# Optimization experiments

Measured on AMD Instinct MI355X. Metric: run time of the kernel, lower is better.

## Reference

```python
import jax, jax.numpy as jnp
import numpy as np

B, C, N, K, OUT = 4, 128, 8192, 20, 128


def setup_inputs() -> dict:
    key = jax.random.key(0)
    k1, k2, k3 = jax.random.split(key, 3)
    x = jax.random.normal(k1, (B, C, N), dtype=jnp.float32)
    W = jax.random.normal(k2, (OUT, 2 * C), dtype=jnp.float32) * 0.02  # 1x1 conv weight over 2C edge channels
    b = jnp.zeros((OUT,), dtype=jnp.float32)
    return {"x": x, "W": W, "b": b}


def _knn_idx(x, k):
    # x: [B, C, N]; pairwise_distance = -||xi - xj||^2 (larger = closer)
    inner = -2.0 * jnp.einsum('bcn,bcm->bnm', x, x)          # [B,N,N]
    xx = jnp.sum(x * x, axis=1)                               # [B,N]
    pd = -xx[:, :, None] - inner - xx[:, None, :]             # [B,N,N]
    return jax.lax.top_k(pd, k)[1]                            # [B,N,k] int32


def reference(x, W, b):
    k = K
    idx = _knn_idx(x, k)                                      # [B,N,k]
    xt = jnp.transpose(x, (0, 2, 1))                          # [B,N,C]
    nbr = jax.vmap(lambda xb, ib: xb[ib])(xt, idx)            # [B,N,k,C] gather
    center = jnp.broadcast_to(xt[:, :, None, :], nbr.shape)   # [B,N,k,C]
    # torch: cat((x, x - feature), dim=3)
    edge = jnp.concatenate([center, center - nbr], axis=-1)   # [B,N,k,2C]
    # 1x1 Conv2d over channel dim + ReLU
    h = jnp.einsum('bnkc,oc->bonk', edge, W) + b[None, :, None, None]
    h = jax.nn.relu(h)
    # aggregate over neighbors (EdgeConv max pooling)
    return jnp.max(h, axis=-1)                                # [B,OUT,N]
```

## Files before the change

kernel.cpp:

```cpp
#include <hip/hip_runtime.h>
#include <float.h>

#define Bz   4
#define Cz   128
#define Nz   8192
#define Kz   20
#define OUTz 128

__global__ __launch_bounds__(256) void xx_kernel(const float* __restrict__ x,
                                                 float* __restrict__ xx) {
    int t = blockIdx.x * 256 + threadIdx.x;
    int b = t >> 13;
    int n = t & (Nz - 1);
    const float* xp = x + (size_t)b * Cz * Nz + n;
    float s = 0.f;
#pragma unroll 8
    for (int c = 0; c < Cz; ++c) {
        float v = xp[(size_t)c * Nz];
        s = fmaf(v, v, s);
    }
    xx[t] = s;
}

__global__ __launch_bounds__(256) void knn_kernel(const float* __restrict__ x,
                                                  const float* __restrict__ xxg,
                                                  int* __restrict__ idxout) {
    const int b  = blockIdx.y;
    const int q0 = blockIdx.x * 32;

    __shared__ __align__(16) float Ald[128 * 32];
    __shared__ __align__(16) float buf2[2 * 8 * 256];
    float* bufA = buf2;
    float* bufB = buf2 + 2048;
    float* sc   = buf2;

    const int tid  = threadIdx.x;
    const int tx   = tid & 31;
    const int ty   = tid >> 5;
    const int lane = tid & 63;
    const int wid  = tid >> 6;

    const float* xb = x + (size_t)b * Cz * Nz;

    {
        int q4 = (tid & 7) * 4;
        int c0 = tid >> 3;
#pragma unroll
        for (int rep = 0; rep < 4; ++rep) {
            int c = c0 + rep * 32;
            *(float4*)&Ald[c * 32 + q4] =
                *(const float4*)&xb[(size_t)c * Nz + q0 + q4];
        }
    }

    float tv[Kz];
    int   ti[Kz];
#pragma unroll
    for (int s = 0; s < Kz; ++s) { tv[s] = -FLT_MAX; ti[s] = 0; }
    float wv = -FLT_MAX;
    int wslot = 0;
    const int orow = wid * 8 + lane;
    const int srow = wid * 8 + (lane & 7);
    const int part = lane >> 3;

    float4 st0[2], st1[2];

#define LOADCHUNK(dst, kj, ch)                                                \
    {                                                                         \
        _Pragma("unroll")                                                     \
        for (int i = 0; i < 2; ++i)                                           \
            dst[i] = *(const float4*)&xb[(size_t)((ch) * 8 + ty) * Nz + (kj) + tx * 4 + i * 128]; \
    }

#define WRITECHUNK(src, buf)                                                  \
    {                                                                         \
        _Pragma("unroll")                                                     \
        for (int i = 0; i < 2; ++i)                                           \
            *(float4*)&(buf)[ty * 256 + tx * 4 + i * 128] = src[i];           \
    }

#define COMPUTECHUNK(buf, ch)                                                 \
    {                                                                         \
        _Pragma("unroll")                                                     \
        for (int cc = 0; cc < 8; ++cc) {                                      \
            float4 a0 = *(const float4*)&Ald[((ch) * 8 + cc) * 32 + ty * 4];  \
            float4 b0 = *(const float4*)&(buf)[cc * 256 + tx * 4];            \
            float4 b1 = *(const float4*)&(buf)[cc * 256 + 128 + tx * 4];      \
            float av[4] = {a0.x, a0.y, a0.z, a0.w};                           \
            float bv[8] = {b0.x, b0.y, b0.z, b0.w, b1.x, b1.y, b1.z, b1.w};   \
            _Pragma("unroll")                                                 \
            for (int q = 0; q < 4; ++q) {                                     \
                _Pragma("unroll")                                             \
                for (int k = 0; k < 8; ++k)                                   \
                    acc[q][k] = fmaf(av[q], bv[k], acc[q][k]);                \
            }                                                                 \
        }                                                                     \
    }

#define EXTRACT(pm_, gbase_)                                                  \
    {                                                                         \
        unsigned long long pm = (pm_);                                        \
        while (pm) {                                                          \
            int j = __ffsll(pm) - 1;                                          \
            pm &= pm - 1;                                                     \
            float s = sc[orow * 64 + ((j + 4 * orow) & 63)];                  \
            if (s > wv) {                                                     \
                int gj = (gbase_) + j;                                        \
                _Pragma("unroll")                                             \
                for (int s2 = 0; s2 < Kz; ++s2) {                             \
                    bool hit = (s2 == wslot);                                 \
                    tv[s2] = hit ? s : tv[s2];                                \
                    ti[s2] = hit ? gj : ti[s2];                               \
                }                                                             \
                wv = tv[0]; wslot = 0;                                        \
                _Pragma("unroll")                                             \
                for (int s2 = 1; s2 < Kz; ++s2)                               \
                    if (tv[s2] < wv) { wv = tv[s2]; wslot = s2; }             \
            }                                                                 \
        }                                                                     \
    }

    LOADCHUNK(st0, 0, 0);

#pragma unroll 1
    for (int kt = 0; kt < Nz / 256; ++kt) {
        const int kj0 = kt * 256;
        const int kjn = ((kt + 1) & (Nz / 256 - 1)) * 256;

        float acc[4][8];
#pragma unroll
        for (int q = 0; q < 4; ++q)
#pragma unroll
            for (int k = 0; k < 8; ++k) acc[q][k] = 0.f;

#pragma unroll 1
        for (int cp = 0; cp < 8; ++cp) {
            const int e = 2 * cp;
            WRITECHUNK(st0, bufA);
            __syncthreads();
            LOADCHUNK(st1, kj0, e + 1);
            COMPUTECHUNK(bufA, e);
            WRITECHUNK(st1, bufB);
            __syncthreads();
            if (e == 14) { LOADCHUNK(st0, kjn, 0); }
            else         { LOADCHUNK(st0, kj0, e + 2); }
            COMPUTECHUNK(bufB, e + 1);
        }
        __syncthreads();

        float4 xxlo = *(const float4*)&xxg[b * Nz + kj0 + tx * 4];
        float4 xxhi = *(const float4*)&xxg[b * Nz + kj0 + 128 + tx * 4];
        float xxa[8] = {xxlo.x, xxlo.y, xxlo.z, xxlo.w,
                        xxhi.x, xxhi.y, xxhi.z, xxhi.w};
        const int txh = tx >> 4;
        const int cl0 = (tx & 15) * 4;

#pragma unroll
        for (int h = 0; h < 4; ++h) {
            if (txh == (h & 1)) {
                const int qs = (h >> 1) * 4;
#pragma unroll
                for (int dq = 0; dq < 4; ++dq) {
                    int r = ty * 4 + dq;
                    float4 w;
                    w.x = 2.f * acc[dq][qs + 0] - xxa[qs + 0];
                    w.y = 2.f * acc[dq][qs + 1] - xxa[qs + 1];
                    w.z = 2.f * acc[dq][qs + 2] - xxa[qs + 2];
                    w.w = 2.f * acc[dq][qs + 3] - xxa[qs + 3];
                    *(float4*)&sc[r * 64 + ((cl0 + 4 * r) & 63)] = w;
                }
            }
            __syncthreads();

            float wvb = __shfl(wv, lane & 7);
            unsigned m = 0;
#pragma unroll
            for (int g = 0; g < 2; ++g) {
                int col = part * 8 + g * 4;
                float4 v = *(const float4*)&sc[srow * 64 + ((col + 4 * srow) & 63)];
                m |= (unsigned)(v.x > wvb) << (4 * g + 0);
                m |= (unsigned)(v.y > wvb) << (4 * g + 1);
                m |= (unsigned)(v.z > wvb) << (4 * g + 2);
                m |= (unsigned)(v.w > wvb) << (4 * g + 3);
            }
            unsigned long long f = (unsigned long long)m << (8 * part);
            f |= __shfl_xor(f, 8);
            f |= __shfl_xor(f, 16);
            f |= __shfl_xor(f, 32);
            if (lane < 8) { EXTRACT(f, kj0 + h * 64); }
            __syncthreads();
        }
    }

    if (lane < 8) {
        size_t base = ((size_t)b * Nz + q0 + orow) * Kz;
#pragma unroll
        for (int s = 0; s < Kz; ++s) idxout[base + s] = ti[s];
    }
#undef LOADCHUNK
#undef WRITECHUNK
#undef COMPUTECHUNK
#undef EXTRACT
}

__global__ __launch_bounds__(256) void feat_kernel(const float* __restrict__ x,
                                                   const float* __restrict__ W,
                                                   const float* __restrict__ bias,
                                                   float* __restrict__ Y) {
    const int gp0 = blockIdx.x * 64;
    const int b   = gp0 >> 13;
    const int n0  = gp0 & (Nz - 1);
    const int o0  = blockIdx.y * 64;

    __shared__ __align__(16) float xt[128 * 64];
    __shared__ __align__(16) float wt[128 * 64];

    const int tid = threadIdx.x;
    const int tx  = tid & 15;
    const int ty  = tid >> 4;

    {
        int li = tid & 63;
        int c0 = tid >> 6;
        const float* xbp = x + (size_t)b * Cz * Nz + n0;
#pragma unroll
        for (int rep = 0; rep < 32; ++rep) {
            int c = c0 + rep * 4;
            xt[c * 64 + li] = xbp[(size_t)c * Nz + li];
        }
    }
    {
        int lo = tid & 63;
        int c0 = tid >> 6;
        int oo = o0 + lo;
#pragma unroll
        for (int rep = 0; rep < 32; ++rep) {
            int c = c0 + rep * 4;
            float w;
            if (oo < 128) w = W[oo * 256 + c] + W[oo * 256 + 128 + c];
            else          w = W[(oo - 128) * 256 + 128 + c];
            wt[c * 64 + lo] = w;
        }
    }
    __syncthreads();

    float acc[4][4];
#pragma unroll
    for (int di = 0; di < 4; ++di)
#pragma unroll
        for (int dj = 0; dj < 4; ++dj) acc[di][dj] = 0.f;

    const int aoff = ty * 4;
    const int boff = tx * 4;
#pragma unroll 8
    for (int c = 0; c < 128; ++c) {
        float4 a  = *(const float4*)&xt[c * 64 + aoff];
        float4 ww = *(const float4*)&wt[c * 64 + boff];
        float av[4] = {a.x, a.y, a.z, a.w};
        float wvv[4] = {ww.x, ww.y, ww.z, ww.w};
#pragma unroll
        for (int di = 0; di < 4; ++di)
#pragma unroll
            for (int dj = 0; dj < 4; ++dj)
                acc[di][dj] = fmaf(av[di], wvv[dj], acc[di][dj]);
    }

    float4 bv = make_float4(0.f, 0.f, 0.f, 0.f);
    if (o0 < 128) bv = *(const float4*)&bias[o0 + tx * 4];
#pragma unroll
    for (int di = 0; di < 4; ++di) {
        float4 r;
        r.x = acc[di][0] + bv.x;
        r.y = acc[di][1] + bv.y;
        r.z = acc[di][2] + bv.z;
        r.w = acc[di][3] + bv.w;
        *(float4*)&Y[(size_t)(gp0 + ty * 4 + di) * 256 + o0 + tx * 4] = r;
    }
}

__global__ __launch_bounds__(256) void gather_kernel(const int* __restrict__ idxg,
                                                     const float* __restrict__ Y,
                                                     float* __restrict__ out) {
    const int gp0 = blockIdx.x * 64;
    const int b   = gp0 >> 13;
    const int n0  = gp0 & (Nz - 1);

    __shared__ int lidx[64 * 21];
    const int tid = threadIdx.x;
    for (int t = tid; t < 64 * Kz; t += 256) {
        int p = t / Kz, j = t - p * Kz;
        lidx[p * 21 + j] = idxg[(size_t)(gp0 + p) * Kz + j];
    }
    __syncthreads();

    const int p  = tid & 63;
    const int o0 = (tid >> 6) * 32;

    float mn[32];
#pragma unroll
    for (int q = 0; q < 32; ++q) mn[q] = FLT_MAX;

    for (int j = 0; j < Kz; ++j) {
        int m = lidx[p * 21 + j];
        const float4* vr =
            (const float4*)(Y + (size_t)(b * Nz + m) * 256 + 128 + o0);
#pragma unroll
        for (int q = 0; q < 8; ++q) {
            float4 v4 = vr[q];
            mn[4 * q + 0] = fminf(mn[4 * q + 0], v4.x);
            mn[4 * q + 1] = fminf(mn[4 * q + 1], v4.y);
            mn[4 * q + 2] = fminf(mn[4 * q + 2], v4.z);
            mn[4 * q + 3] = fminf(mn[4 * q + 3], v4.w);
        }
    }

    const float4* ur = (const float4*)(Y + (size_t)(gp0 + p) * 256 + o0);
#pragma unroll
    for (int q = 0; q < 8; ++q) {
        float4 u4 = ur[q];
        float r0 = fmaxf(u4.x - mn[4 * q + 0], 0.f);
        float r1 = fmaxf(u4.y - mn[4 * q + 1], 0.f);
        float r2 = fmaxf(u4.z - mn[4 * q + 2], 0.f);
        float r3 = fmaxf(u4.w - mn[4 * q + 3], 0.f);
        size_t ob = ((size_t)b * OUTz + o0 + 4 * q) * Nz + n0 + p;
        out[ob + 0 * Nz] = r0;
        out[ob + 1 * Nz] = r1;
        out[ob + 2 * Nz] = r2;
        out[ob + 3 * Nz] = r3;
    }
}

extern "C" void kernel_launch(void* const* d_in, const int* in_sizes, int n_in,
                              void* d_out, int out_size, void* d_ws, size_t ws_size,
                              hipStream_t stream) {
    const float* x    = (const float*)d_in[0];
    const float* W    = (const float*)d_in[1];
    const float* bias = (const float*)d_in[2];
    float* out = (float*)d_out;

    char* ws = (char*)d_ws;
    float* xx  = (float*)ws;
    int*   idx = (int*)(ws + (1 << 17));
    float* Y   = (float*)(ws + (4 << 20));

    xx_kernel<<<dim3(Bz * Nz / 256), dim3(256), 0, stream>>>(x, xx);

    knn_kernel<<<dim3(Nz / 32, Bz), dim3(256), 0, stream>>>(x, xx, idx);

    feat_kernel<<<dim3(Bz * Nz / 64, 4), dim3(256), 0, stream>>>(x, W, bias, Y);

    gather_kernel<<<dim3(Bz * Nz / 64), dim3(256), 0, stream>>>(idx, Y, out);
}
```

Before: 1.579 ms.

## Stream query features via scalar loads and compute distances per-thread without LDS tiling

Rewrites the kNN distance GEMM so each thread owns one key and accumulates dot products against all 32 queries. Query values are fetched into scalar registers with inline s_load_dwordx16, double-buffered across channels, and key values are loaded straight from global memory into VGPRs. This removes the LDS staging buffers and the per-chunk __syncthreads, and moves operand broadcast onto the scalar unit. In exchange each query value is now used for only one FMA per thread, reuse of key loads is lost, the inline asm waitcnt scheduling is fragile, and register pressure rises.

```diff
diff --git a/kernel.cpp b/kernel.cpp
--- a/kernel.cpp
+++ b/kernel.cpp
@@ -6,6 +6,8 @@
 #define Nz   8192
 #define Kz   20
 #define OUTz 128
+
+typedef float f16v __attribute__((ext_vector_type(16)));
 
 __global__ __launch_bounds__(256) void xx_kernel(const float* __restrict__ x,
                                                  float* __restrict__ xx) {
@@ -28,30 +30,14 @@
     const int b  = blockIdx.y;
     const int q0 = blockIdx.x * 32;
 
-    __shared__ __align__(16) float Ald[128 * 32];
-    __shared__ __align__(16) float buf2[2 * 8 * 256];
-    float* bufA = buf2;
-    float* bufB = buf2 + 2048;
-    float* sc   = buf2;
+    __shared__ float sc[32 * 64];
 
     const int tid  = threadIdx.x;
-    const int tx   = tid & 31;
-    const int ty   = tid >> 5;
     const int lane = tid & 63;
     const int wid  = tid >> 6;
 
     const float* xb = x + (size_t)b * Cz * Nz;
-
-    {
-        int q4 = (tid & 7) * 4;
-        int c0 = tid >> 3;
-#pragma unroll
-        for (int rep = 0; rep < 4; ++rep) {
-            int c = c0 + rep * 32;
-            *(float4*)&Ald[c * 32 + q4] =
-                *(const float4*)&xb[(size_t)c * Nz + q0 + q4];
-        }
-    }
+    const float* aq = xb + q0;
 
     float tv[Kz];
     int   ti[Kz];
@@ -63,39 +49,35 @@
     const int srow = wid * 8 + (lane & 7);
     const int part = lane >> 3;
 
-    float4 st0[2], st1[2];
-
-#define LOADCHUNK(dst, kj, ch)                                                \
+    f16v sA0, sB0, sA1, sB1;
+    asm volatile("s_load_dwordx16 %0, %2, 0x0\n\t"
+                 "s_load_dwordx16 %1, %2, 0x40"
+                 : "=&s"(sA0), "=&s"(sB0) : "s"(aq));
+
+#define CSTEP(cA, cB, nA, nB, vbv, cidx)                                      \
     {                                                                         \
+        const int cn_ = ((cidx) + 1) & 127;                                   \
+        const float* apn_ = aq + ((size_t)cn_ << 13);                         \
+        asm volatile("s_waitcnt lgkmcnt(0)" : "+s"(cA), "+s"(cB));            \
+        asm volatile("s_load_dwordx16 %0, %2, 0x0\n\t"                        \
+                     "s_load_dwordx16 %1, %2, 0x40"                           \
+                     : "=&s"(nA), "=&s"(nB) : "s"(apn_));                     \
+        const float vv_ = (vbv);                                              \
         _Pragma("unroll")                                                     \
-        for (int i = 0; i < 2; ++i)                                           \
-            dst[i] = *(const float4*)&xb[(size_t)((ch) * 8 + ty) * Nz + (kj) + tx * 4 + i * 128]; \
-    }
-
-#define WRITECHUNK(src, buf)                                                  \
-    {                                                                         \
+        for (int q = 0; q < 16; ++q) acc[q] = fmaf(cA[q], vv_, acc[q]);       \
         _Pragma("unroll")                                                     \
-        for (int i = 0; i < 2; ++i)                                           \
-            *(float4*)&(buf)[ty * 256 + tx * 4 + i * 128] = src[i];           \
-    }
-
-#define COMPUTECHUNK(buf, ch)                                                 \
-    {                                                                         \
-        _Pragma("unroll")                                                     \
-        for (int cc = 0; cc < 8; ++cc) {                                      \
-            float4 a0 = *(const float4*)&Ald[((ch) * 8 + cc) * 32 + ty * 4];  \
-            float4 b0 = *(const float4*)&(buf)[cc * 256 + tx * 4];            \
-            float4 b1 = *(const float4*)&(buf)[cc * 256 + 128 + tx * 4];      \
-            float av[4] = {a0.x, a0.y, a0.z, a0.w};                           \
-            float bv[8] = {b0.x, b0.y, b0.z, b0.w, b1.x, b1.y, b1.z, b1.w};   \
-            _Pragma("unroll")                                                 \
-            for (int q = 0; q < 4; ++q) {                                     \
-                _Pragma("unroll")                                             \
-                for (int k = 0; k < 8; ++k)                                   \
-                    acc[q][k] = fmaf(av[q], bv[k], acc[q][k]);                \
-            }                                                                 \
-        }                                                                     \
-    }
+        for (int q = 0; q < 16; ++q) acc[16 + q] = fmaf(cB[q], vv_, acc[16 + q]); \
+    }
+
+#define GROUP8(vb, cb)                                                        \
+    CSTEP(sA0, sB0, sA1, sB1, vb[0], (cb) + 0)                                \
+    CSTEP(sA1, sB1, sA0, sB0, vb[1], (cb) + 1)                                \
+    CSTEP(sA0, sB0, sA1, sB1, vb[2], (cb) + 2)                                \
+    CSTEP(sA1, sB1, sA0, sB0, vb[3], (cb) + 3)                                \
+    CSTEP(sA0, sB0, sA1, sB1, vb[4], (cb) + 4)                                \
+    CSTEP(sA1, sB1, sA0, sB0, vb[5], (cb) + 5)                                \
+    CSTEP(sA0, sB0, sA1, sB1, vb[6], (cb) + 6)                                \
+    CSTEP(sA1, sB1, sA0, sB0, vb[7], (cb) + 7)
 
 #define EXTRACT(pm_, gbase_)                                                  \
     {                                                                         \
@@ -120,55 +102,43 @@
         }                                                                     \
     }
 
-    LOADCHUNK(st0, 0, 0);
-
 #pragma unroll 1
-    for (int kt = 0; kt < Nz / 256; ++kt) {
-        const int kj0 = kt * 256;
-        const int kjn = ((kt + 1) & (Nz / 256 - 1)) * 256;
-
-        float acc[4][8];
-#pragma unroll
-        for (int q = 0; q < 4; ++q)
-#pragma unroll
-            for (int k = 0; k < 8; ++k) acc[q][k] = 0.f;
+    for (int kp = 0; kp < Nz / 256; ++kp) {
+        const int key = kp * 256 + tid;
+        const float* bp = xb + key;
+
+        float acc[32];
+#pragma unroll
+        for (int q = 0; q < 32; ++q) acc[q] = 0.f;
+
+        float vbE[8], vbO[8];
+#pragma unroll
+        for (int i = 0; i < 8; ++i) vbE[i] = bp[(size_t)i * Nz];
 
 #pragma unroll 1
-        for (int cp = 0; cp < 8; ++cp) {
-            const int e = 2 * cp;
-            WRITECHUNK(st0, bufA);
-            __syncthreads();
-            LOADCHUNK(st1, kj0, e + 1);
-            COMPUTECHUNK(bufA, e);
-            WRITECHUNK(st1, bufB);
-            __syncthreads();
-            if (e == 14) { LOADCHUNK(st0, kjn, 0); }
-            else         { LOADCHUNK(st0, kj0, e + 2); }
-            COMPUTECHUNK(bufB, e + 1);
-        }
-        __syncthreads();
-
-        float4 xxlo = *(const float4*)&xxg[b * Nz + kj0 + tx * 4];
-        float4 xxhi = *(const float4*)&xxg[b * Nz + kj0 + 128 + tx * 4];
-        float xxa[8] = {xxlo.x, xxlo.y, xxlo.z, xxlo.w,
-                        xxhi.x, xxhi.y, xxhi.z, xxhi.w};
-        const int txh = tx >> 4;
-        const int cl0 = (tx & 15) * 4;
-
-#pragma unroll
-        for (int h = 0; h < 4; ++h) {
-            if (txh == (h & 1)) {
-                const int qs = (h >> 1) * 4;
-#pragma unroll
-                for (int dq = 0; dq < 4; ++dq) {
-                    int r = ty * 4 + dq;
-                    float4 w;
-                    w.x = 2.f * acc[dq][qs + 0] - xxa[qs + 0];
-                    w.y = 2.f * acc[dq][qs + 1] - xxa[qs + 1];
-                    w.z = 2.f * acc[dq][qs + 2] - xxa[qs + 2];
-                    w.w = 2.f * acc[dq][qs + 3] - xxa[qs + 3];
-                    *(float4*)&sc[r * 64 + ((cl0 + 4 * r) & 63)] = w;
-                }
+        for (int gp = 0; gp < 8; ++gp) {
+            {
+                const float* bg = bp + ((size_t)(2 * gp + 1) << 3) * Nz;
+#pragma unroll
+                for (int i = 0; i < 8; ++i) vbO[i] = bg[(size_t)i * Nz];
+            }
+            GROUP8(vbE, gp * 16)
+            {
+                const int gn = (2 * gp + 2) & 15;
+                const float* bg = bp + ((size_t)gn << 3) * Nz;
+#pragma unroll
+                for (int i = 0; i < 8; ++i) vbE[i] = bg[(size_t)i * Nz];
+            }
+            GROUP8(vbO, gp * 16 + 8)
+        }
+
+        const float xxk = xxg[b * Nz + key];
+#pragma unroll
+        for (int sp = 0; sp < 4; ++sp) {
+            if (wid == sp) {
+#pragma unroll
+                for (int q = 0; q < 32; ++q)
+                    sc[q * 64 + ((lane + 4 * q) & 63)] = 2.f * acc[q] - xxk;
             }
             __syncthreads();
 
@@ -187,7 +157,7 @@
             f |= __shfl_xor(f, 8);
             f |= __shfl_xor(f, 16);
             f |= __shfl_xor(f, 32);
-            if (lane < 8) { EXTRACT(f, kj0 + h * 64); }
+            if (lane < 8) { EXTRACT(f, kp * 256 + sp * 64); }
             __syncthreads();
         }
     }
@@ -197,9 +167,8 @@
 #pragma unroll
         for (int s = 0; s < Kz; ++s) idxout[base + s] = ti[s];
     }
-#undef LOADCHUNK
-#undef WRITECHUNK
-#undef COMPUTECHUNK
+#undef CSTEP
+#undef GROUP8
 #undef EXTRACT
 }
 
```

Measured after the change: 1.689 ms. +7.0%, slower.
